# Optimization experiments

Measured on AMD Instinct MI355X. Metric: run time of the kernel, lower is better.

## Reference

```python
import jax, jax.numpy as jnp
import numpy as np

FACTOR = 3   # ProbAttention factor hardcoded in Informer.__init__
N_HEADS = 8


def _ln(x, g, b, eps=1e-5):
    m = x.mean(-1, keepdims=True)
    v = ((x - m) ** 2).mean(-1, keepdims=True)
    return (x - m) / jnp.sqrt(v + eps) * g + b


def _pos_emb(L, d_model):
    # standard fixed sinusoidal positional embedding (Informer PositionalEmbedding)
    pos = np.arange(L, dtype=np.float32)[:, None]
    div = np.exp(np.arange(0, d_model, 2, dtype=np.float32) * (-np.log(10000.0) / d_model))
    pe = np.zeros((L, d_model), np.float32)
    pe[:, 0::2] = np.sin(pos * div)
    pe[:, 1::2] = np.cos(pos * div)
    return jnp.asarray(pe)


def _prob_attention(q, k, v, rng_key):
    # q,k,v: [B, L, H, D]; mask_flag=False, scale=None -> 1/sqrt(D)
    B, L, H, D = q.shape
    Q = q.transpose(0, 2, 1, 3)
    K = k.transpose(0, 2, 1, 3)
    V = v.transpose(0, 2, 1, 3)
    L_Q = L_K = L
    U_part = min(FACTOR * int(np.ceil(np.log(L_K))), L_K)   # sampled keys per query
    u = min(FACTOR * int(np.ceil(np.log(L_Q))), L_Q)        # top queries kept
    # sample keys (shared across batch/heads, as in torch.randint(L_K,(L_Q,sample_k)))
    idx_sample = jax.random.randint(rng_key, (L_Q, U_part), 0, L_K)
    K_sample = K[:, :, idx_sample, :]                        # [B,H,L_Q,U_part,D]
    QK_sample = jnp.einsum('bhld,bhlsd->bhls', Q, K_sample)  # [B,H,L_Q,U_part]
    M = QK_sample.max(-1) - QK_sample.sum(-1) / L_K          # sparsity measure [B,H,L_Q]
    _, idx_top = jax.lax.top_k(M, u)                         # [B,H,u]
    Q_reduce = jnp.take_along_axis(Q, idx_top[..., None], axis=2)          # [B,H,u,D]
    scores = jnp.einsum('bhud,bhkd->bhuk', Q_reduce, K) / jnp.sqrt(jnp.float32(D))
    attn = jax.nn.softmax(scores, axis=-1)
    upd = jnp.einsum('bhuk,bhkd->bhud', attn, V)             # [B,H,u,D]
    # initial context = mean over values (mask_flag=False), overwrite at top queries
    ctx = jnp.broadcast_to(V.mean(axis=2, keepdims=True), (B, H, L_Q, D))
    bI = jnp.arange(B)[:, None, None]
    hI = jnp.arange(H)[None, :, None]
    ctx = ctx.at[bI, hI, idx_top].set(upd)
    return ctx.transpose(0, 2, 1, 3).reshape(B, L, H * D)


def _forward(x, time_features, g_in, b_in, W_tok, W_time, b_time,
             Wq, bq, Wk, bk, Wv, bv, Wo, bo, W1, b1, W2, b2,
             g1, be1, g2, be2, g_enc, b_enc, W_pre, b_pre, W_fc, b_fc):
    B, L, _ = x.shape
    d_model = W_tok.shape[-1]
    H = N_HEADS
    D = d_model // H
    x = _ln(x, g_in, b_in)                                   # input_norm over enc_in
    # DataEmbedding: circular Conv1d(k=3) token emb + positional + timeF linear
    xp = jnp.pad(x, ((0, 0), (1, 1), (0, 0)), mode='wrap')
    tok = jax.lax.conv_general_dilated(xp, W_tok, (1,), 'VALID',
                                       dimension_numbers=('NWC', 'WIO', 'NWC'))
    h = tok + _pos_emb(L, d_model)[None] + time_features @ W_time.T + b_time
    key = jax.random.key(42)
    for i in range(Wq.shape[0]):                              # e_layers (small, fixed)
        q = (h @ Wq[i].T + bq[i]).reshape(B, L, H, D)
        k = (h @ Wk[i].T + bk[i]).reshape(B, L, H, D)
        v = (h @ Wv[i].T + bv[i]).reshape(B, L, H, D)
        attn_out = _prob_attention(q, k, v, jax.random.fold_in(key, i))
        h = h + attn_out @ Wo[i].T + bo[i]
        h = _ln(h, g1[i], be1[i])
        y = jax.nn.relu(h @ W1[i].T + b1[i]) @ W2[i].T + b2[i]  # 1x1 convs == linears
        h = _ln(h + y, g2[i], be2[i])
    h = _ln(h, g_enc, b_enc)
    last = h[:, -1, :]
    return jax.nn.relu(last @ W_pre.T + b_pre) @ W_fc.T + b_fc


def setup_inputs() -> dict:
    key = jax.random.key(0)
    B, L, C_IN, DM, DFF, E = 8, 2048, 32, 512, 2048, 2
    ks = iter(jax.random.split(key, 48))

    def p(shape, s=0.02):
        return jax.random.normal(next(ks), shape, jnp.float32) * s

    return {
        'x': jax.random.normal(next(ks), (B, L, C_IN), jnp.float32),
        'time_features': jax.random.uniform(next(ks), (B, L, 4), jnp.float32),
        'g_in': jnp.ones((C_IN,), jnp.float32), 'b_in': jnp.zeros((C_IN,), jnp.float32),
        'W_tok': p((3, C_IN, DM)),
        'W_time': p((DM, 4)), 'b_time': jnp.zeros((DM,), jnp.float32),
        'Wq': p((E, DM, DM)), 'bq': jnp.zeros((E, DM), jnp.float32),
        'Wk': p((E, DM, DM)), 'bk': jnp.zeros((E, DM), jnp.float32),
        'Wv': p((E, DM, DM)), 'bv': jnp.zeros((E, DM), jnp.float32),
        'Wo': p((E, DM, DM)), 'bo': jnp.zeros((E, DM), jnp.float32),
        'W1': p((E, DFF, DM)), 'b1': jnp.zeros((E, DFF), jnp.float32),
        'W2': p((E, DM, DFF)), 'b2': jnp.zeros((E, DM), jnp.float32),
        'g1': jnp.ones((E, DM), jnp.float32), 'be1': jnp.zeros((E, DM), jnp.float32),
        'g2': jnp.ones((E, DM), jnp.float32), 'be2': jnp.zeros((E, DM), jnp.float32),
        'g_enc': jnp.ones((DM,), jnp.float32), 'b_enc': jnp.zeros((DM,), jnp.float32),
        'W_pre': p((DM // 2, DM)), 'b_pre': jnp.zeros((DM // 2,), jnp.float32),
        'W_fc': p((1, DM // 2)), 'b_fc': jnp.zeros((1,), jnp.float32),
    }


def reference(x, time_features, g_in, b_in, W_tok, W_time, b_time,
              Wq, bq, Wk, bk, Wv, bv, Wo, bo, W1, b1, W2, b2,
              g1, be1, g2, be2, g_enc, b_enc, W_pre, b_pre, W_fc, b_fc):
    return _forward(x, time_features, g_in, b_in, W_tok, W_time, b_time,
                    Wq, bq, Wk, bk, Wv, bv, Wo, bo, W1, b1, W2, b2,
                    g1, be1, g2, be2, g_enc, b_enc, W_pre, b_pre, W_fc, b_fc)
```

## Files before the change

### kernel.cpp

```cpp
#include <hip/hip_runtime.h>
#include <math.h>

#define BATCH 8
#define SEQ   2048
#define TOK   (BATCH*SEQ)
#define CIN   32
#define DM    512
#define DFF   2048
#define NH    8
#define HD    64
#define NSAMP 24
#define NTOP  24
#define NSLAB 8
#define EPS   1e-5f
#define QKVLD 1536

typedef unsigned int u32;
typedef unsigned short u16;
typedef unsigned long long u64;
typedef __attribute__((ext_vector_type(8))) short short8;
typedef __attribute__((ext_vector_type(4))) short short4v;
typedef __attribute__((ext_vector_type(4))) float floatx4;

__device__ __forceinline__ void async16(const void* g, void* l) {
    __builtin_amdgcn_global_load_lds((const __attribute__((address_space(1))) u32*)g,
                                     (__attribute__((address_space(3))) u32*)l, 16, 0, 0);
}
__device__ __forceinline__ u16 bf16rn(float f) {
    u32 u = __float_as_uint(f);
    return (u16)((u + 0x7fffu + ((u >> 16) & 1u)) >> 16);
}
__device__ __forceinline__ void sep_store(u16* base, size_t row, int ld2, int j, float v) {
    u16 hb = bf16rn(v);
    float r = v - __uint_as_float((u32)hb << 16);
    size_t o = row * (size_t)ld2 + (size_t)((j >> 3) << 4) + (j & 7);
    base[o] = hb;
    base[o + 8] = bf16rn(r);
}
__device__ __forceinline__ float sep_load(const u16* base, size_t row, int ld2, int j) {
    size_t o = row * (size_t)ld2 + (size_t)((j >> 3) << 4) + (j & 7);
    return __uint_as_float((u32)base[o] << 16) + __uint_as_float((u32)base[o + 8] << 16);
}
__device__ __forceinline__ float hl2f(u16 h, u16 l) {
    return __uint_as_float((u32)h << 16) + __uint_as_float((u32)l << 16);
}

__device__ __forceinline__ void tf_round(unsigned &x0, unsigned &x1, int r) {
    x0 += x1;
    x1 = (x1 << r) | (x1 >> (32 - r));
    x1 ^= x0;
}
__device__ __forceinline__ void threefry(unsigned k0, unsigned k1,
                                         unsigned c0, unsigned c1,
                                         unsigned &o0, unsigned &o1) {
    unsigned ks0 = k0, ks1 = k1, ks2 = k0 ^ k1 ^ 0x1BD11BDAu;
    unsigned x0 = c0 + ks0, x1 = c1 + ks1;
    tf_round(x0,x1,13); tf_round(x0,x1,15); tf_round(x0,x1,26); tf_round(x0,x1,6);
    x0 += ks1; x1 += ks2 + 1u;
    tf_round(x0,x1,17); tf_round(x0,x1,29); tf_round(x0,x1,16); tf_round(x0,x1,24);
    x0 += ks2; x1 += ks0 + 2u;
    tf_round(x0,x1,13); tf_round(x0,x1,15); tf_round(x0,x1,26); tf_round(x0,x1,6);
    x0 += ks0; x1 += ks1 + 3u;
    tf_round(x0,x1,17); tf_round(x0,x1,29); tf_round(x0,x1,16); tf_round(x0,x1,24);
    x0 += ks1; x1 += ks2 + 4u;
    tf_round(x0,x1,13); tf_round(x0,x1,15); tf_round(x0,x1,26); tf_round(x0,x1,6);
    x0 += ks2; x1 += ks0 + 5u;
    o0 = x0; o1 = x1;
}

__global__ void sample_kernel(int* __restrict__ idx_sample) {
    const int HALF = (SEQ * NSAMP) / 2;
    int p = blockIdx.x * blockDim.x + threadIdx.x;
    int li = blockIdx.y;
    if (p >= HALF) return;
    unsigned f0, f1;
    threefry(0u, 42u, 0u, (unsigned)li, f0, f1);
    unsigned a0, a1, b0, b1;
    threefry(f0, f1, 0u, 2u, a0, a1);
    threefry(f0, f1, 1u, 3u, b0, b1);
    unsigned o0, o1;
    threefry(a1, b1, (unsigned)p, (unsigned)(p + HALF), o0, o1);
    idx_sample[li * SEQ * NSAMP + p]        = (int)(o0 & (SEQ - 1));
    idx_sample[li * SEQ * NSAMP + p + HALF] = (int)(o1 & (SEQ - 1));
}

__global__ __launch_bounds__(256) void ln_in_kernel(const float* __restrict__ x,
        const float* __restrict__ g, const float* __restrict__ b,
        float* __restrict__ out) {
    int t = blockIdx.x * blockDim.x + threadIdx.x;
    if (t >= TOK) return;
    const float* xr = x + (size_t)t * CIN;
    float vals[CIN];
    float s = 0.f;
#pragma unroll
    for (int c = 0; c < CIN; c++) { vals[c] = xr[c]; s += vals[c]; }
    float m = s * (1.f / CIN);
    float v = 0.f;
#pragma unroll
    for (int c = 0; c < CIN; c++) { float d = vals[c] - m; v += d * d; }
    v *= (1.f / CIN);
    float inv = rsqrtf(v + EPS);
    float* orow = out + (size_t)t * CIN;
#pragma unroll
    for (int c = 0; c < CIN; c++) orow[c] = (vals[c] - m) * inv * g[c] + b[c];
}

__global__ __launch_bounds__(128) void im2col_kernel(const float* __restrict__ xln,
        u16* __restrict__ a) {
    int t = blockIdx.x;
    int j = threadIdx.x;
    if (j >= 96) return;
    int b = t >> 11, l = t & 2047;
    int w = j >> 5, c = j & 31;
    int lw = (l - 1 + w + SEQ) & 2047;
    sep_store(a, (size_t)t, 192, j, xln[(((size_t)b << 11) | lw) * CIN + c]);
}

__global__ __launch_bounds__(256) void wtok_split(const float* __restrict__ Wtok,
        u16* __restrict__ wt) {
    int e = blockIdx.x * 256 + threadIdx.x;
    int o = e / 96, j = e % 96;
    sep_store(wt, (size_t)o, 192, j, Wtok[(size_t)j * DM + o]);
}

__global__ __launch_bounds__(256) void pe_kernel(float* __restrict__ pe) {
    int e = blockIdx.x * 256 + threadIdx.x;
    int l = e >> 9, o = e & 511;
    const float c1 = -0.017988946039016f;
    int i2 = o & ~1;
    float div = expf((float)i2 * c1);
    float arg = (float)l * div;
    pe[e] = (o & 1) ? cosf(arg) : sinf(arg);
}

__global__ __launch_bounds__(256) void rsd_kernel(const float* __restrict__ pe,
        const float* __restrict__ tfeat, const float* __restrict__ Wtime,
        u16* __restrict__ rsd) {
    int t = blockIdx.x, tid = threadIdx.x;
    int l = t & 2047;
    float t0 = tfeat[(size_t)t * 4], t1 = tfeat[(size_t)t * 4 + 1];
    float t2 = tfeat[(size_t)t * 4 + 2], t3 = tfeat[(size_t)t * 4 + 3];
    for (int o = tid; o < DM; o += 256) {
        float v = pe[l * DM + o]
            + t0 * Wtime[o * 4] + t1 * Wtime[o * 4 + 1]
            + t2 * Wtime[o * 4 + 2] + t3 * Wtime[o * 4 + 3];
        sep_store(rsd, (size_t)t, 1024, o, v);
    }
}

__global__ __launch_bounds__(256) void split_weights(const float* __restrict__ Wq,
        const float* __restrict__ Wk, const float* __restrict__ Wv,
        const float* __restrict__ Wo, const float* __restrict__ W1,
        const float* __restrict__ W2, u16* __restrict__ out,
        const float* __restrict__ bq, const float* __restrict__ bk,
        const float* __restrict__ bv, float* __restrict__ bqkv) {
    int i = blockIdx.x * 256 + threadIdx.x;
    if (i < 1536)
        bqkv[i] = (i < 512) ? bq[i] : (i < 1024) ? bk[i - 512] : bv[i - 1024];
    if (i < 1048576) {
        const float* src = (i < 262144) ? Wq : (i < 524288) ? Wk : (i < 786432) ? Wv : Wo;
        int off = i & 262143;
        size_t base = (size_t)(i >> 18) * 524288;
        sep_store(out + base, (size_t)(off >> 9), 1024, off & 511, src[off]);
    } else if (i < 2097152) {
        int off = i - 1048576;
        sep_store(out + 2097152, (size_t)(off >> 9), 1024, off & 511, W1[off]);
    } else {
        int off = i - 2097152;
        sep_store(out + 4194304, (size_t)(off >> 11), 4096, off & 2047, W2[off]);
    }
}

template<bool RELU, bool RESP, bool OUTP, bool OUTB>
__global__ __launch_bounds__(256, 2) void gemm_pp(const u16* __restrict__ Ap,
        const u16* __restrict__ Wp, const float* __restrict__ bias,
        const u16* __restrict__ RsdS, float* __restrict__ Cf, u16* __restrict__ Cp,
        int ldc, int K, int lda) {
    __shared__ alignas(16) u16 At[2][8192];
    __shared__ alignas(16) u16 Wt[2][8192];
    const int tid = threadIdx.x;
    int linear = blockIdx.y * gridDim.x + blockIdx.x;
    int xcd = linear & 7, sseq = linear >> 3;
    int mper = gridDim.y >> 3;
    int mt = xcd * mper + (sseq % mper);
    int nt = sseq / mper;
    const int m0 = mt * 128, n0 = nt * 128;
    const int lane = tid & 63, wv = tid >> 6;
    const int wm = wv >> 1, wn = wv & 1;
    const int fr = lane & 15, q = lane >> 4;

    floatx4 acc[4][4] = {};

    const int r0 = tid >> 3;
    const int gc = (tid & 7) ^ (r0 & 7);
    const u16* abase = Ap + (size_t)(m0 + r0) * (2 * lda) + gc * 8;
    const u16* wbase = Wp + (size_t)(n0 + r0) * (2 * K) + gc * 8;
    const size_t astep = (size_t)32 * 2 * lda;
    const size_t wstep = (size_t)32 * 2 * K;
    const int doff = tid * 16;
    const int nk = K >> 5;

    const int cph = ((q << 1) ^ (fr & 7)) << 3;
    const int cpl = ((q << 1) ^ (fr & 7) ^ 1) << 3;

#pragma unroll
    for (int i = 0; i < 4; i++) {
        async16(abase + i * astep, (char*)At[0] + doff + i * 4096);
        async16(wbase + i * wstep, (char*)Wt[0] + doff + i * 4096);
    }

    for (int k = 0; k < nk; k++) {
        const int b = k & 1;
        __syncthreads();
        if (k + 1 < nk) {
            int k2 = (k + 1) << 6;
#pragma unroll
            for (int i = 0; i < 4; i++) {
                async16(abase + k2 + i * astep, (char*)At[b ^ 1] + doff + i * 4096);
                async16(wbase + k2 + i * wstep, (char*)Wt[b ^ 1] + doff + i * 4096);
            }
        }
        short8 ah[4], al[4];
#pragma unroll
        for (int mi = 0; mi < 4; mi++) {
            int r = wm * 64 + mi * 16 + fr;
            ah[mi] = *(const short8*)&At[b][r * 64 + cph];
            al[mi] = *(const short8*)&At[b][r * 64 + cpl];
        }
#pragma unroll
        for (int ni = 0; ni < 4; ni++) {
            int r = wn * 64 + ni * 16 + fr;
            short8 wh8 = *(const short8*)&Wt[b][r * 64 + cph];
            short8 wl8 = *(const short8*)&Wt[b][r * 64 + cpl];
#pragma unroll
            for (int mi = 0; mi < 4; mi++) {
                acc[mi][ni] = __builtin_amdgcn_mfma_f32_16x16x32_bf16(ah[mi], wh8, acc[mi][ni], 0, 0, 0);
                acc[mi][ni] = __builtin_amdgcn_mfma_f32_16x16x32_bf16(ah[mi], wl8, acc[mi][ni], 0, 0, 0);
                acc[mi][ni] = __builtin_amdgcn_mfma_f32_16x16x32_bf16(al[mi], wh8, acc[mi][ni], 0, 0, 0);
            }
        }
    }
#pragma unroll
    for (int ni = 0; ni < 4; ni++) {
        int col = n0 + wn * 64 + ni * 16 + fr;
        float bv = bias[col];
#pragma unroll
        for (int mi = 0; mi < 4; mi++) {
            int row = m0 + wm * 64 + mi * 16 + q * 4;
#pragma unroll
            for (int r = 0; r < 4; r++) {
                float v = acc[mi][ni][r] + bv;
                if (RESP) v += sep_load(RsdS, (size_t)(row + r), 2 * ldc, col);
                if (RELU) v = fmaxf(v, 0.f);
                if (OUTP)      sep_store(Cp, (size_t)(row + r), 2 * ldc, col, v);
                else if (OUTB) Cp[(size_t)(row + r) * ldc + col] = bf16rn(v);
                else           Cf[(size_t)(row + r) * ldc + col] = v;
            }
        }
    }
}

template<bool RELU, bool RESP>
__global__ __launch_bounds__(256, 2) void gemm_sb(const u16* __restrict__ Ab,
        const u16* __restrict__ Wp, const float* __restrict__ bias,
        const u16* __restrict__ RsdS, float* __restrict__ Cf,
        int ldc, int K, int lda) {
    __shared__ alignas(16) u16 At[2][4096];
    __shared__ alignas(16) u16 Wt[2][8192];
    const int tid = threadIdx.x;
    int linear = blockIdx.y * gridDim.x + blockIdx.x;
    int xcd = linear & 7, sseq = linear >> 3;
    int mper = gridDim.y >> 3;
    int mt = xcd * mper + (sseq % mper);
    int nt = sseq / mper;
    const int m0 = mt * 128, n0 = nt * 128;
    const int lane = tid & 63, wv = tid >> 6;
    const int wm = wv >> 1, wn = wv & 1;
    const int fr = lane & 15, q = lane >> 4;

    floatx4 acc[4][4] = {};

    const int ar = tid & 127;
    const u16* abase = Ab + (size_t)(m0 + ar) * lda + (tid >> 7) * 8;
    const int adoff = tid * 16;
    const int r0 = tid >> 3;
    const int gc = (tid & 7) ^ (r0 & 7);
    const u16* wbase = Wp + (size_t)(n0 + r0) * (2 * K) + gc * 8;
    const size_t wstep = (size_t)32 * 2 * K;
    const int wdoff = tid * 16;
    const int nk = K >> 5;

    const int cph = ((q << 1) ^ (fr & 7)) << 3;
    const int cpl = ((q << 1) ^ (fr & 7) ^ 1) << 3;

#pragma unroll
    for (int i = 0; i < 2; i++)
        async16(abase + i * 16, (char*)At[0] + adoff + i * 4096);
#pragma unroll
    for (int i = 0; i < 4; i++)
        async16(wbase + i * wstep, (char*)Wt[0] + wdoff + i * 4096);

    for (int k = 0; k < nk; k++) {
        const int b = k & 1;
        __syncthreads();
        if (k + 1 < nk) {
            int ka = (k + 1) << 5;
            int kw = (k + 1) << 6;
#pragma unroll
            for (int i = 0; i < 2; i++)
                async16(abase + ka + i * 16, (char*)At[b ^ 1] + adoff + i * 4096);
#pragma unroll
            for (int i = 0; i < 4; i++)
                async16(wbase + kw + i * wstep, (char*)Wt[b ^ 1] + wdoff + i * 4096);
        }
        short8 af[4];
#pragma unroll
        for (int mi = 0; mi < 4; mi++) {
            int r = wm * 64 + mi * 16 + fr;
            af[mi] = *(const short8*)&At[b][q * 1024 + r * 8];
        }
#pragma unroll
        for (int ni = 0; ni < 4; ni++) {
            int r = wn * 64 + ni * 16 + fr;
            short8 wh8 = *(const short8*)&Wt[b][r * 64 + cph];
            short8 wl8 = *(const short8*)&Wt[b][r * 64 + cpl];
#pragma unroll
            for (int mi = 0; mi < 4; mi++) {
                acc[mi][ni] = __builtin_amdgcn_mfma_f32_16x16x32_bf16(af[mi], wh8, acc[mi][ni], 0, 0, 0);
                acc[mi][ni] = __builtin_amdgcn_mfma_f32_16x16x32_bf16(af[mi], wl8, acc[mi][ni], 0, 0, 0);
            }
        }
    }
#pragma unroll
    for (int ni = 0; ni < 4; ni++) {
        int col = n0 + wn * 64 + ni * 16 + fr;
        float bv = bias[col];
#pragma unroll
        for (int mi = 0; mi < 4; mi++) {
            int row = m0 + wm * 64 + mi * 16 + q * 4;
#pragma unroll
            for (int r = 0; r < 4; r++) {
                float v = acc[mi][ni][r] + bv;
                if (RESP) v += sep_load(RsdS, (size_t)(row + r), 2 * ldc, col);
                if (RELU) v = fmaxf(v, 0.f);
                Cf[(size_t)(row + r) * ldc + col] = v;
            }
        }
    }
}

__global__ __launch_bounds__(256) void qk_sample_kernel(const float* __restrict__ qkv,
        const int* __restrict__ idx_sample, float* __restrict__ Mout) {
    int r = (blockIdx.x * 256 + threadIdx.x) >> 6;
    int lane = threadIdx.x & 63;
    if (r >= BATCH * NH * SEQ) return;
    int b = r / (NH * SEQ);
    int head = (r / SEQ) % NH;
    int l = r % SEQ;
    int sidx = lane >> 4, dc = lane & 15;
    const float* qrow = qkv + ((size_t)(b * SEQ + l)) * QKVLD + head * HD + dc * 4;
    float4 qf = *(const float4*)qrow;
    int myidx = (lane < NSAMP) ? idx_sample[l * NSAMP + lane] : 0;
    const float* kbase = qkv + (size_t)b * SEQ * QKVLD + 512 + head * HD + dc * 4;
    int kidx[6];
#pragma unroll
    for (int p = 0; p < 6; p++) kidx[p] = __shfl(myidx, p * 4 + sidx);
    float4 kf[6];
#pragma unroll
    for (int p = 0; p < 6; p++) kf[p] = *(const float4*)(kbase + (size_t)kidx[p] * QKVLD);
    float mx = -INFINITY, sm = 0.f;
#pragma unroll
    for (int p = 0; p < 6; p++) {
        float part = qf.x * kf[p].x + qf.y * kf[p].y + qf.z * kf[p].z + qf.w * kf[p].w;
        part += __shfl_xor(part, 1);
        part += __shfl_xor(part, 2);
        part += __shfl_xor(part, 4);
        part += __shfl_xor(part, 8);
        mx = fmaxf(mx, part);
        sm += part;
    }
    mx = fmaxf(mx, __shfl_xor(mx, 16));
    mx = fmaxf(mx, __shfl_xor(mx, 32));
    sm += __shfl_xor(sm, 16);
    sm += __shfl_xor(sm, 32);
    if (lane == 0) Mout[r] = mx - sm * (1.f / SEQ);
}

__device__ __forceinline__ u64 pack_key(float v, int idx) {
    u32 u = __float_as_uint(v);
    u32 m = (u & 0x80000000u) ? ~u : (u | 0x80000000u);
    return ((u64)m << 32) | (u32)(~(u32)idx);
}

__global__ __launch_bounds__(256) void topk_part(const float* __restrict__ Mbuf,
        u64* __restrict__ cand) {
    __shared__ u64 wred[4];
    int bh = blockIdx.x, chunk = blockIdx.y;
    int tid = threadIdx.x, wv = tid >> 6, lane = tid & 63;
    int l = chunk * 256 + tid;
    u64 val = pack_key(Mbuf[(size_t)bh * SEQ + l], l);
    for (int it = 0; it < NTOP; it++) {
        u64 w = val;
#pragma unroll
        for (int off = 32; off > 0; off >>= 1) {
            u64 o = __shfl_xor(w, off);
            if (o > w) w = o;
        }
        if (lane == 0) wred[wv] = w;
        __syncthreads();
        u64 win = wred[0];
        if (wred[1] > win) win = wred[1];
        if (wred[2] > win) win = wred[2];
        if (wred[3] > win) win = wred[3];
        if (val == win) val = 0;
        if (tid == 0) cand[((size_t)bh * 8 + chunk) * NTOP + it] = win;
        __syncthreads();
    }
}

__global__ __launch_bounds__(256) void topk_merge(const u64* __restrict__ cand,
        int* __restrict__ idx_top) {
    __shared__ u64 wred[4];
    int bh = blockIdx.x;
    int tid = threadIdx.x, wv = tid >> 6, lane = tid & 63;
    u64 val = (tid < 8 * NTOP) ? cand[(size_t)bh * 8 * NTOP + tid] : 0;
    for (int it = 0; it < NTOP; it++) {
        u64 w = val;
#pragma unroll
        for (int off = 32; off > 0; off >>= 1) {
            u64 o = __shfl_xor(w, off);
            if (o > w) w = o;
        }
        if (lane == 0) wred[wv] = w;
        __syncthreads();
        u64 win = wred[0];
        if (wred[1] > win) win = wred[1];
        if (wred[2] > win) win = wred[2];
        if (wred[3] > win) win = wred[3];
        if (val == win) val = 0;
        if (tid == 0) idx_top[bh * NTOP + it] = (int)(~(u32)(win & 0xffffffffull) & (SEQ - 1));
        __syncthreads();
    }
}

__global__ __launch_bounds__(256) void vmean_kernel(const float* __restrict__ qkv,
        float* __restrict__ vmean) {
    __shared__ float red[256];
    int bh = blockIdx.x, slab = blockIdx.y;
    int b = bh >> 3, head = bh & 7;
    int seg = threadIdx.x >> 6, d = threadIdx.x & 63;
    int base_row = slab * 256 + seg * 64;
    float s = 0.f;
    for (int r = 0; r < 64; r++)
        s += qkv[((size_t)(b * SEQ + base_row + r)) * QKVLD + 1024 + head * HD + d];
    red[threadIdx.x] = s;
    __syncthreads();
    if (threadIdx.x < 128) red[threadIdx.x] += red[threadIdx.x + 128];
    __syncthreads();
    if (threadIdx.x < 64) {
        float t = red[threadIdx.x] + red[threadIdx.x + 64];
        atomicAdd(&vmean[bh * HD + d], t * (1.f / SEQ));
    }
}

__global__ __launch_bounds__(512) void ydef_kernel(const float* __restrict__ Wo,
        const float* __restrict__ bo, const float* __restrict__ vmean,
        float* __restrict__ ydef) {
    __shared__ float vm[DM];
    int b = blockIdx.x, o = threadIdx.x;
    vm[o] = vmean[b * DM + o];
    __syncthreads();
    const float* wr = Wo + (size_t)o * DM;
    float acc = bo[o];
    for (int j = 0; j < DM; j += 4) {
        float4 w4 = *(const float4*)&wr[j];
        acc += w4.x * vm[j] + w4.y * vm[j + 1] + w4.z * vm[j + 2] + w4.w * vm[j + 3];
    }
    ydef[b * DM + o] = acc;
}

__global__ __launch_bounds__(256) void resid_kernel(const u16* __restrict__ hp,
        const float* __restrict__ ydef, float* __restrict__ hf) {
    int wv = threadIdx.x >> 6, lane = threadIdx.x & 63;
    int t = blockIdx.x * 4 + wv;
    int b = t >> 11;
    const u16* sp = hp + (size_t)t * 1024 + (lane >> 1) * 16 + (lane & 1) * 4;
    short4v h0 = *(const short4v*)sp;
    short4v l0 = *(const short4v*)(sp + 8);
    short4v h1 = *(const short4v*)(sp + 512);
    short4v l1 = *(const short4v*)(sp + 520);
    int j0 = (lane >> 1) * 8 + (lane & 1) * 4;
    const float* yd = ydef + b * DM;
    float4 y0 = *(const float4*)&yd[j0];
    float4 y1 = *(const float4*)&yd[j0 + 256];
    float4 o0, o1;
    o0.x = hl2f((u16)h0[0], (u16)l0[0]) + y0.x;
    o0.y = hl2f((u16)h0[1], (u16)l0[1]) + y0.y;
    o0.z = hl2f((u16)h0[2], (u16)l0[2]) + y0.z;
    o0.w = hl2f((u16)h0[3], (u16)l0[3]) + y0.w;
    o1.x = hl2f((u16)h1[0], (u16)l1[0]) + y1.x;
    o1.y = hl2f((u16)h1[1], (u16)l1[1]) + y1.y;
    o1.z = hl2f((u16)h1[2], (u16)l1[2]) + y1.z;
    o1.w = hl2f((u16)h1[3], (u16)l1[3]) + y1.w;
    *(float4*)&hf[(size_t)t * DM + j0] = o0;
    *(float4*)&hf[(size_t)t * DM + j0 + 256] = o1;
}

__global__ __launch_bounds__(512) void corr_kernel(const float* __restrict__ Wo,
        const float* __restrict__ updC, const float* __restrict__ vmean,
        const int* __restrict__ idx_top, float* __restrict__ hf) {
    __shared__ float delta[NTOP][HD];
    __shared__ int rows[NTOP];
    int bh = blockIdx.x, b = bh >> 3, h = bh & 7;
    int tid = threadIdx.x;
    for (int i = tid; i < NTOP * HD; i += 512) {
        int u = i >> 6, d = i & 63;
        delta[u][d] = updC[((size_t)bh * NTOP + u) * HD + d] - vmean[bh * HD + d];
    }
    if (tid < NTOP) rows[tid] = idx_top[bh * NTOP + tid];
    __syncthreads();
    float w[HD];
    const float* wr = Wo + (size_t)tid * DM + h * HD;
#pragma unroll
    for (int d = 0; d < HD; d += 4) {
        float4 f = *(const float4*)&wr[d];
        w[d] = f.x; w[d + 1] = f.y; w[d + 2] = f.z; w[d + 3] = f.w;
    }
    for (int u = 0; u < NTOP; u++) {
        float acc = 0.f;
#pragma unroll
        for (int d = 0; d < HD; d++) acc += w[d] * delta[u][d];
        atomicAdd(&hf[(size_t)(b * SEQ + rows[u]) * DM + tid], acc);
    }
}

__global__ __launch_bounds__(256) void spattn_flash(const float* __restrict__ qkv,
        const int* __restrict__ idx_top, float* __restrict__ opart,
        float* __restrict__ mspart) {
    __shared__ float KtT[64][65];
    __shared__ float Vt[64][65];
    __shared__ float Qs[24][64];
    __shared__ float Ps[24][66];
    int bh = blockIdx.x, slab = blockIdx.y;
    int b = bh >> 3, h = bh & 7;
    int tid = threadIdx.x;
    int wv = tid >> 6, lane = tid & 63;
    for (int i = tid; i < NTOP * 64; i += 256) {
        int u = i >> 6, d = i & 63;
        int qi = idx_top[bh * NTOP + u];
        Qs[u][d] = qkv[((size_t)(b * SEQ + qi)) * QKVLD + h * HD + d];
    }
    float m[6], s[6], o[6], alpha[6];
#pragma unroll
    for (int j = 0; j < 6; j++) { m[j] = -INFINITY; s[j] = 0.f; o[j] = 0.f; }
    int key0 = slab * (SEQ / NSLAB);
    int sr = tid >> 2, sc0 = (tid & 3) * 16;
    for (int t = 0; t < (SEQ / NSLAB) / 64; t++) {
        int kbase = key0 + t * 64;
        __syncthreads();
        const float* kr = qkv + ((size_t)(b * SEQ + kbase + sr)) * QKVLD + 512 + h * HD + sc0;
        const float* vr = qkv + ((size_t)(b * SEQ + kbase + sr)) * QKVLD + 1024 + h * HD + sc0;
        float kf[16], vf[16];
        *(float4*)&kf[0]  = *(const float4*)(kr);
        *(float4*)&kf[4]  = *(const float4*)(kr + 4);
        *(float4*)&kf[8]  = *(const float4*)(kr + 8);
        *(float4*)&kf[12] = *(const float4*)(kr + 12);
        *(float4*)&vf[0]  = *(const float4*)(vr);
        *(float4*)&vf[4]  = *(const float4*)(vr + 4);
        *(float4*)&vf[8]  = *(const float4*)(vr + 8);
        *(float4*)&vf[12] = *(const float4*)(vr + 12);
#pragma unroll
        for (int i = 0; i < 16; i++) {
            KtT[sc0 + i][sr] = kf[i];
            Vt[sr][sc0 + i] = vf[i];
        }
        __syncthreads();
        float dot[6] = {};
#pragma unroll
        for (int d = 0; d < 64; d++) {
            float kv = KtT[d][lane];
#pragma unroll
            for (int j = 0; j < 6; j++) dot[j] += Qs[wv * 6 + j][d] * kv;
        }
#pragma unroll
        for (int j = 0; j < 6; j++) {
            float sc = dot[j] * 0.125f;
            float tmax = sc;
            for (int off = 32; off > 0; off >>= 1) tmax = fmaxf(tmax, __shfl_xor(tmax, off));
            float mn = fmaxf(m[j], tmax);
            float p = __expf(sc - mn);
            float psum = p;
            for (int off = 32; off > 0; off >>= 1) psum += __shfl_xor(psum, off);
            alpha[j] = __expf(m[j] - mn);
            s[j] = s[j] * alpha[j] + psum;
            m[j] = mn;
            Ps[wv * 6 + j][lane] = p;
        }
        float pv[6] = {};
#pragma unroll
        for (int key = 0; key < 64; key++) {
            float vvv = Vt[key][lane];
#pragma unroll
            for (int j = 0; j < 6; j++) pv[j] += Ps[wv * 6 + j][key] * vvv;
        }
#pragma unroll
        for (int j = 0; j < 6; j++) o[j] = o[j] * alpha[j] + pv[j];
    }
    float* ob = opart + ((size_t)(bh * NSLAB + slab)) * NTOP * 64;
#pragma unroll
    for (int j = 0; j < 6; j++) ob[(wv * 6 + j) * 64 + lane] = o[j];
    if (lane == 0) {
        float* ms = mspart + ((size_t)(bh * NSLAB + slab)) * NTOP * 2;
#pragma unroll
        for (int j = 0; j < 6; j++) {
            ms[(wv * 6 + j) * 2]     = m[j];
            ms[(wv * 6 + j) * 2 + 1] = s[j];
        }
    }
}

__global__ __launch_bounds__(256) void spattn_combine(const float* __restrict__ opart,
        const float* __restrict__ mspart, float* __restrict__ updC) {
    __shared__ float wgt[NSLAB][NTOP];
    int bh = blockIdx.x;
    int tid = threadIdx.x;
    if (tid < NTOP) {
        float mv[NSLAB], sv[NSLAB];
        float M = -INFINITY;
#pragma unroll
        for (int sl = 0; sl < NSLAB; sl++) {
            mv[sl] = mspart[((size_t)(bh * NSLAB + sl)) * NTOP * 2 + tid * 2];
            sv[sl] = mspart[((size_t)(bh * NSLAB + sl)) * NTOP * 2 + tid * 2 + 1];
            M = fmaxf(M, mv[sl]);
        }
        float S = 0.f;
#pragma unroll
        for (int sl = 0; sl < NSLAB; sl++) S += sv[sl] * __expf(mv[sl] - M);
        float invS = 1.f / S;
#pragma unroll
        for (int sl = 0; sl < NSLAB; sl++) wgt[sl][tid] = __expf(mv[sl] - M) * invS;
    }
    __syncthreads();
    for (int i = tid; i < NTOP * 64; i += 256) {
        int u = i >> 6, d = i & 63;
        float val = 0.f;
#pragma unroll
        for (int sl = 0; sl < NSLAB; sl++)
            val += wgt[sl][u] * opart[(((size_t)(bh * NSLAB + sl)) * NTOP + u) * 64 + d];
        updC[((size_t)bh * NTOP + u) * 64 + d] = val;
    }
}

template<bool INP, bool OUTSEP>
__global__ __launch_bounds__(256) void ln_kernel(const float* __restrict__ srcF,
        const u16* __restrict__ srcS, const float* __restrict__ g,
        const float* __restrict__ b, float* __restrict__ dstF, u16* __restrict__ dstS) {
    int wv = threadIdx.x >> 6, lane = threadIdx.x & 63;
    int t = blockIdx.x * 4 + wv;
    float xv[8];
    if (INP) {
        const u16* sp = srcS + (size_t)t * 1024 + (lane >> 1) * 16 + (lane & 1) * 4;
        short4v h0 = *(const short4v*)sp;
        short4v l0 = *(const short4v*)(sp + 8);
        short4v h1 = *(const short4v*)(sp + 512);
        short4v l1 = *(const short4v*)(sp + 520);
#pragma unroll
        for (int i = 0; i < 4; i++) {
            xv[i]     = hl2f((u16)h0[i], (u16)l0[i]);
            xv[i + 4] = hl2f((u16)h1[i], (u16)l1[i]);
        }
    } else {
        float4 x0 = *(const float4*)&srcF[(size_t)t * DM + lane * 4];
        float4 x1 = *(const float4*)&srcF[(size_t)t * DM + lane * 4 + 256];
        xv[0] = x0.x; xv[1] = x0.y; xv[2] = x0.z; xv[3] = x0.w;
        xv[4] = x1.x; xv[5] = x1.y; xv[6] = x1.z; xv[7] = x1.w;
    }
    float s = 0.f, s2 = 0.f;
#pragma unroll
    for (int i = 0; i < 8; i++) { s += xv[i]; s2 += xv[i] * xv[i]; }
#pragma unroll
    for (int off = 32; off > 0; off >>= 1) {
        s  += __shfl_xor(s, off);
        s2 += __shfl_xor(s2, off);
    }
    float m = s * (1.f / DM);
    float var = s2 * (1.f / DM) - m * m;
    float inv = rsqrtf(var + EPS);
    float4 g0 = *(const float4*)&g[lane * 4];
    float4 g1 = *(const float4*)&g[lane * 4 + 256];
    float4 b0 = *(const float4*)&b[lane * 4];
    float4 b1 = *(const float4*)&b[lane * 4 + 256];
    float y[8];
    y[0] = (xv[0] - m) * inv * g0.x + b0.x;  y[1] = (xv[1] - m) * inv * g0.y + b0.y;
    y[2] = (xv[2] - m) * inv * g0.z + b0.z;  y[3] = (xv[3] - m) * inv * g0.w + b0.w;
    y[4] = (xv[4] - m) * inv * g1.x + b1.x;  y[5] = (xv[5] - m) * inv * g1.y + b1.y;
    y[6] = (xv[6] - m) * inv * g1.z + b1.z;  y[7] = (xv[7] - m) * inv * g1.w + b1.w;
    if (OUTSEP) {
        u16* dp = dstS + (size_t)t * 1024 + (lane >> 1) * 16 + (lane & 1) * 4;
        short4v hh0, ll0, hh1, ll1;
#pragma unroll
        for (int i = 0; i < 4; i++) {
            u16 hb = bf16rn(y[i]);
            hh0[i] = (short)hb;
            ll0[i] = (short)bf16rn(y[i] - __uint_as_float((u32)hb << 16));
            u16 hb2 = bf16rn(y[i + 4]);
            hh1[i] = (short)hb2;
            ll1[i] = (short)bf16rn(y[i + 4] - __uint_as_float((u32)hb2 << 16));
        }
        *(short4v*)dp = hh0;
        *(short4v*)(dp + 8) = ll0;
        *(short4v*)(dp + 512) = hh1;
        *(short4v*)(dp + 520) = ll1;
    } else {
        float4 o0 = { y[0], y[1], y[2], y[3] };
        float4 o1 = { y[4], y[5], y[6], y[7] };
        *(float4*)&dstF[(size_t)t * DM + lane * 4] = o0;
        *(float4*)&dstF[(size_t)t * DM + lane * 4 + 256] = o1;
    }
}

__global__ __launch_bounds__(256) void head_kernel(const float* __restrict__ hfin,
        const float* __restrict__ Wpre, const float* __restrict__ bpre,
        const float* __restrict__ Wfc, const float* __restrict__ bfc,
        float* __restrict__ out) {
    __shared__ float last[DM];
    __shared__ float red[256];
    int b = blockIdx.x, tid = threadIdx.x;
    const float* hr = hfin + ((size_t)(b * SEQ + SEQ - 1)) * DM;
    last[tid] = hr[tid];
    last[tid + 256] = hr[tid + 256];
    __syncthreads();
    float acc = bpre[tid];
    for (int c = 0; c < DM; c++) acc += last[c] * Wpre[tid * DM + c];
    acc = fmaxf(acc, 0.f);
    red[tid] = acc * Wfc[tid];
    __syncthreads();
    for (int s = 128; s > 0; s >>= 1) { if (tid < s) red[tid] += red[tid + s]; __syncthreads(); }
    if (tid == 0) out[b] = red[0] + bfc[0];
}

extern "C" void kernel_launch(void* const* d_in, const int* in_sizes, int n_in,
                              void* d_out, int out_size, void* d_ws, size_t ws_size,
                              hipStream_t stream) {
    (void)in_sizes; (void)n_in; (void)out_size; (void)ws_size;
    const float* x      = (const float*)d_in[0];
    const float* tfeat  = (const float*)d_in[1];
    const float* g_in   = (const float*)d_in[2];
    const float* b_in   = (const float*)d_in[3];
    const float* W_tok  = (const float*)d_in[4];
    const float* W_time = (const float*)d_in[5];
    const float* b_time = (const float*)d_in[6];
    const float* Wq     = (const float*)d_in[7];
    const float* bq     = (const float*)d_in[8];
    const float* Wk     = (const float*)d_in[9];
    const float* bk     = (const float*)d_in[10];
    const float* Wv     = (const float*)d_in[11];
    const float* bv     = (const float*)d_in[12];
    const float* Wo     = (const float*)d_in[13];
    const float* bo     = (const float*)d_in[14];
    const float* W1     = (const float*)d_in[15];
    const float* b1     = (const float*)d_in[16];
    const float* W2     = (const float*)d_in[17];
    const float* b2     = (const float*)d_in[18];
    const float* g1     = (const float*)d_in[19];
    const float* be1    = (const float*)d_in[20];
    const float* g2     = (const float*)d_in[21];
    const float* be2    = (const float*)d_in[22];
    const float* g_enc  = (const float*)d_in[23];
    const float* b_enc  = (const float*)d_in[24];
    const float* W_pre  = (const float*)d_in[25];
    const float* b_pre  = (const float*)d_in[26];
    const float* W_fc   = (const float*)d_in[27];
    const float* b_fc   = (const float*)d_in[28];
    float* out = (float*)d_out;

    char* ws = (char*)d_ws;
    u16*   hp   = (u16*)(ws);
    float* hf   = (float*)(ws + 33554432);
    char*  bigc = ws + 67108864;
    float* qkv  = (float*)bigc;
    u16*   midP = (u16*)bigc;
    u16*   midB = (u16*)bigc;
    float* updC   = (float*)(bigc + 100663296);
    float* ydefb  = (float*)(bigc + 101056512);
    float* opart  = (float*)(bigc + 101072896);
    float* mspart = (float*)(bigc + 104218624);
    float* xln  = (float*)(bigc);
    u16*   acvP = (u16*)(bigc + 2097152);
    float* pe   = (float*)(bigc + 8388608);
    u16*   rsdS = (u16*)(bigc + 12582912);
    u16*   wtok = (u16*)(bigc + 46137344);
    u16*   wsep       = (u16*)(ws + 201326592);
    float* Mbuf       = (float*)(ws + 213909504);
    float* vmean      = (float*)(ws + 214433792);
    int*   idx_sample = (int*)(ws + 214450176);
    int*   idx_top    = (int*)(ws + 214843392);
    float* biasqkv    = (float*)(ws + 214849536);
    u64*   cand       = (u64*)(ws + 214855680);

    ln_in_kernel<<<TOK / 256, 256, 0, stream>>>(x, g_in, b_in, xln);
    im2col_kernel<<<TOK, 128, 0, stream>>>(xln, acvP);
    wtok_split<<<192, 256, 0, stream>>>(W_tok, wtok);
    pe_kernel<<<4096, 256, 0, stream>>>(pe);
    rsd_kernel<<<TOK, 256, 0, stream>>>(pe, tfeat, W_time, rsdS);
    sample_kernel<<<dim3(96, 2), 256, 0, stream>>>(idx_sample);

    gemm_pp<false, true, true, false><<<dim3(4, 128), 256, 0, stream>>>(
        acvP, wtok, b_time, rsdS, nullptr, hp, DM, 96, 96);

    const u16* wqkv_p = wsep;
    const u16* w1_p = wsep + 2097152;
    const u16* w2_p = wsep + 4194304;

    for (int li = 0; li < 2; li++) {
        split_weights<<<12288, 256, 0, stream>>>(
            Wq + (size_t)li * DM * DM, Wk + (size_t)li * DM * DM,
            Wv + (size_t)li * DM * DM, Wo + (size_t)li * DM * DM,
            W1 + (size_t)li * DFF * DM, W2 + (size_t)li * DM * DFF, wsep,
            bq + (size_t)li * DM, bk + (size_t)li * DM, bv + (size_t)li * DM, biasqkv);

        const float* Wo_i = Wo + (size_t)li * DM * DM;
        const float* bo_i = bo + (size_t)li * DM;
        const float* b1_i = b1 + (size_t)li * DFF;
        const float* b2_i = b2 + (size_t)li * DM;
        const float* g1_i = g1 + (size_t)li * DM;
        const float* be1_i = be1 + (size_t)li * DM;
        const float* g2_i = g2 + (size_t)li * DM;
        const float* be2_i = be2 + (size_t)li * DM;

        gemm_pp<false, false, false, false><<<dim3(QKVLD / 128, TOK / 128), 256, 0, stream>>>(
            hp, wqkv_p, biasqkv, nullptr, qkv, nullptr, QKVLD, DM, DM);

        qk_sample_kernel<<<(BATCH * NH * SEQ) / 4, 256, 0, stream>>>(
            qkv, idx_sample + li * SEQ * NSAMP, Mbuf);
        topk_part<<<dim3(BATCH * NH, 8), 256, 0, stream>>>(Mbuf, cand);
        topk_merge<<<BATCH * NH, 256, 0, stream>>>(cand, idx_top);
        hipMemsetAsync(vmean, 0, BATCH * NH * HD * sizeof(float), stream);
        vmean_kernel<<<dim3(BATCH * NH, 8), 256, 0, stream>>>(qkv, vmean);
        ydef_kernel<<<BATCH, 512, 0, stream>>>(Wo_i, bo_i, vmean, ydefb);
        spattn_flash<<<dim3(BATCH * NH, NSLAB), 256, 0, stream>>>(qkv, idx_top, opart, mspart);
        spattn_combine<<<BATCH * NH, 256, 0, stream>>>(opart, mspart, updC);

        resid_kernel<<<TOK / 4, 256, 0, stream>>>(hp, ydefb, hf);
        corr_kernel<<<BATCH * NH, 512, 0, stream>>>(Wo_i, updC, vmean, idx_top, hf);
        ln_kernel<false, true><<<TOK / 4, 256, 0, stream>>>(hf, nullptr, g1_i, be1_i, nullptr, hp);

        if (li == 0) {
            gemm_pp<true, false, true, false><<<dim3(DFF / 128, TOK / 128), 256, 0, stream>>>(
                hp, w1_p, b1_i, nullptr, nullptr, midP, DFF, DM, DM);
            gemm_pp<false, true, false, false><<<dim3(DM / 128, TOK / 128), 256, 0, stream>>>(
                midP, w2_p, b2_i, hp, hf, nullptr, DM, DFF, DFF);
        } else {
            gemm_pp<true, false, false, true><<<dim3(DFF / 128, TOK / 128), 256, 0, stream>>>(
                hp, w1_p, b1_i, nullptr, nullptr, midB, DFF, DM, DM);
            gemm_sb<false, true><<<dim3(DM / 128, TOK / 128), 256, 0, stream>>>(
                midB, w2_p, b2_i, hp, hf, DM, DFF, DFF);
        }
        ln_kernel<false, true><<<TOK / 4, 256, 0, stream>>>(hf, nullptr, g2_i, be2_i, nullptr, hp);
    }

    ln_kernel<true, false><<<TOK / 4, 256, 0, stream>>>(nullptr, hp, g_enc, b_enc, hf, nullptr);
    head_kernel<<<BATCH, 256, 0, stream>>>(hf, W_pre, b_pre, W_fc, b_fc, out);
}
```

Measured before the change: 1.131 ms.

## Fuse residual, sparse-attention correction and LayerNorm; fold V-mean into attention kernel

Merges the input LayerNorm and im2col into one warp-shuffle kernel. Computes the V mean inside the sparse flash-attention kernel instead of a separate pass over V. Replaces the resid, atomic corr and LayerNorm kernels with one fused pass driven by a per-token head mask and top-query map, which avoids the hf round trip and the atomics. This adds bookkeeping buffers and a memset, and the fused LayerNorm uses the one-pass variance formula, which is less numerically robust.

```diff
diff --git a/kernel.cpp b/kernel.cpp
--- a/kernel.cpp
+++ b/kernel.cpp
@@ -84,36 +84,27 @@
     idx_sample[li * SEQ * NSAMP + p + HALF] = (int)(o1 & (SEQ - 1));
 }
 
-__global__ __launch_bounds__(256) void ln_in_kernel(const float* __restrict__ x,
-        const float* __restrict__ g, const float* __restrict__ b,
-        float* __restrict__ out) {
-    int t = blockIdx.x * blockDim.x + threadIdx.x;
-    if (t >= TOK) return;
-    const float* xr = x + (size_t)t * CIN;
-    float vals[CIN];
-    float s = 0.f;
-#pragma unroll
-    for (int c = 0; c < CIN; c++) { vals[c] = xr[c]; s += vals[c]; }
-    float m = s * (1.f / CIN);
-    float v = 0.f;
-#pragma unroll
-    for (int c = 0; c < CIN; c++) { float d = vals[c] - m; v += d * d; }
-    v *= (1.f / CIN);
-    float inv = rsqrtf(v + EPS);
-    float* orow = out + (size_t)t * CIN;
-#pragma unroll
-    for (int c = 0; c < CIN; c++) orow[c] = (vals[c] - m) * inv * g[c] + b[c];
-}
-
-__global__ __launch_bounds__(128) void im2col_kernel(const float* __restrict__ xln,
-        u16* __restrict__ a) {
-    int t = blockIdx.x;
-    int j = threadIdx.x;
-    if (j >= 96) return;
-    int b = t >> 11, l = t & 2047;
-    int w = j >> 5, c = j & 31;
-    int lw = (l - 1 + w + SEQ) & 2047;
-    sep_store(a, (size_t)t, 192, j, xln[(((size_t)b << 11) | lw) * CIN + c]);
+__global__ __launch_bounds__(256) void ln_im2col_kernel(const float* __restrict__ x,
+        const float* __restrict__ g, const float* __restrict__ b, u16* __restrict__ a) {
+    int sub = threadIdx.x >> 5;
+    int c   = threadIdx.x & 31;
+    int t = blockIdx.x * 8 + sub;
+    int bb = t >> 11, l = t & 2047;
+    float v = x[(size_t)t * CIN + c];
+    float s = v;
+#pragma unroll
+    for (int m = 1; m <= 16; m <<= 1) s += __shfl_xor(s, m);
+    float mean = s * (1.f / CIN);
+    float d = v - mean;
+    float vv = d * d;
+#pragma unroll
+    for (int m = 1; m <= 16; m <<= 1) vv += __shfl_xor(vv, m);
+    float inv = rsqrtf(vv * (1.f / CIN) + EPS);
+    float y = d * inv * g[c] + b[c];
+    size_t base = (size_t)(bb << 11);
+    sep_store(a, base + ((l + 1) & 2047), 192, c, y);
+    sep_store(a, base + l,                192, 32 + c, y);
+    sep_store(a, base + ((l - 1) & 2047), 192, 64 + c, y);
 }
 
 __global__ __launch_bounds__(256) void wtok_split(const float* __restrict__ Wtok,
@@ -419,7 +410,7 @@
 }
 
 __global__ __launch_bounds__(256) void topk_merge(const u64* __restrict__ cand,
-        int* __restrict__ idx_top) {
+        int* __restrict__ idx_top, u32* __restrict__ headmask, u16* __restrict__ umap) {
     __shared__ u64 wred[4];
     int bh = blockIdx.x;
     int tid = threadIdx.x, wv = tid >> 6, lane = tid & 63;
@@ -438,28 +429,13 @@
         if (wred[2] > win) win = wred[2];
         if (wred[3] > win) win = wred[3];
         if (val == win) val = 0;
-        if (tid == 0) idx_top[bh * NTOP + it] = (int)(~(u32)(win & 0xffffffffull) & (SEQ - 1));
+        if (tid == 0) {
+            int row = (int)(~(u32)(win & 0xffffffffull) & (SEQ - 1));
+            idx_top[bh * NTOP + it] = row;
+            umap[(size_t)bh * SEQ + row] = (u16)it;
+            atomicOr(&headmask[(((bh >> 3) << 11) | row)], 1u << (bh & 7));
+        }
         __syncthreads();
-    }
-}
-
-__global__ __launch_bounds__(256) void vmean_kernel(const float* __restrict__ qkv,
-        float* __restrict__ vmean) {
-    __shared__ float red[256];
-    int bh = blockIdx.x, slab = blockIdx.y;
-    int b = bh >> 3, head = bh & 7;
-    int seg = threadIdx.x >> 6, d = threadIdx.x & 63;
-    int base_row = slab * 256 + seg * 64;
-    float s = 0.f;
-    for (int r = 0; r < 64; r++)
-        s += qkv[((size_t)(b * SEQ + base_row + r)) * QKVLD + 1024 + head * HD + d];
-    red[threadIdx.x] = s;
-    __syncthreads();
-    if (threadIdx.x < 128) red[threadIdx.x] += red[threadIdx.x + 128];
-    __syncthreads();
-    if (threadIdx.x < 64) {
-        float t = red[threadIdx.x] + red[threadIdx.x + 64];
-        atomicAdd(&vmean[bh * HD + d], t * (1.f / SEQ));
     }
 }
 
@@ -479,68 +455,115 @@
     ydef[b * DM + o] = acc;
 }
 
-__global__ __launch_bounds__(256) void resid_kernel(const u16* __restrict__ hp,
-        const float* __restrict__ ydef, float* __restrict__ hf) {
+__global__ __launch_bounds__(512) void corrRow_kernel(const float* __restrict__ Wo,
+        const float* __restrict__ updC, const float* __restrict__ vmean,
+        float* __restrict__ corrRow) {
+    __shared__ float delta[NTOP][HD];
+    int bh = blockIdx.x, h = bh & 7;
+    int tid = threadIdx.x;
+    for (int i = tid; i < NTOP * HD; i += 512) {
+        int u = i >> 6, d = i & 63;
+        delta[u][d] = updC[((size_t)bh * NTOP + u) * HD + d] - vmean[bh * HD + d];
+    }
+    __syncthreads();
+    float w[HD];
+    const float* wr = Wo + (size_t)tid * DM + h * HD;
+#pragma unroll
+    for (int d = 0; d < HD; d += 4) {
+        float4 f = *(const float4*)&wr[d];
+        w[d] = f.x; w[d + 1] = f.y; w[d + 2] = f.z; w[d + 3] = f.w;
+    }
+    for (int u = 0; u < NTOP; u++) {
+        float acc = 0.f;
+#pragma unroll
+        for (int d = 0; d < HD; d++) acc += w[d] * delta[u][d];
+        corrRow[((size_t)bh * NTOP + u) * DM + tid] = acc;
+    }
+}
+
+__global__ __launch_bounds__(256) void resid_corr_ln(const u16* __restrict__ hp,
+        const float* __restrict__ ydef, const float* __restrict__ corrRow,
+        const u32* __restrict__ headmask, const u16* __restrict__ umap,
+        const float* __restrict__ g, const float* __restrict__ b,
+        u16* __restrict__ dstS) {
     int wv = threadIdx.x >> 6, lane = threadIdx.x & 63;
     int t = blockIdx.x * 4 + wv;
-    int b = t >> 11;
+    int bb = t >> 11, l = t & 2047;
     const u16* sp = hp + (size_t)t * 1024 + (lane >> 1) * 16 + (lane & 1) * 4;
     short4v h0 = *(const short4v*)sp;
     short4v l0 = *(const short4v*)(sp + 8);
     short4v h1 = *(const short4v*)(sp + 512);
     short4v l1 = *(const short4v*)(sp + 520);
     int j0 = (lane >> 1) * 8 + (lane & 1) * 4;
-    const float* yd = ydef + b * DM;
+    const float* yd = ydef + bb * DM;
     float4 y0 = *(const float4*)&yd[j0];
     float4 y1 = *(const float4*)&yd[j0 + 256];
-    float4 o0, o1;
-    o0.x = hl2f((u16)h0[0], (u16)l0[0]) + y0.x;
-    o0.y = hl2f((u16)h0[1], (u16)l0[1]) + y0.y;
-    o0.z = hl2f((u16)h0[2], (u16)l0[2]) + y0.z;
-    o0.w = hl2f((u16)h0[3], (u16)l0[3]) + y0.w;
-    o1.x = hl2f((u16)h1[0], (u16)l1[0]) + y1.x;
-    o1.y = hl2f((u16)h1[1], (u16)l1[1]) + y1.y;
-    o1.z = hl2f((u16)h1[2], (u16)l1[2]) + y1.z;
-    o1.w = hl2f((u16)h1[3], (u16)l1[3]) + y1.w;
-    *(float4*)&hf[(size_t)t * DM + j0] = o0;
-    *(float4*)&hf[(size_t)t * DM + j0 + 256] = o1;
-}
-
-__global__ __launch_bounds__(512) void corr_kernel(const float* __restrict__ Wo,
-        const float* __restrict__ updC, const float* __restrict__ vmean,
-        const int* __restrict__ idx_top, float* __restrict__ hf) {
-    __shared__ float delta[NTOP][HD];
-    __shared__ int rows[NTOP];
-    int bh = blockIdx.x, b = bh >> 3, h = bh & 7;
-    int tid = threadIdx.x;
-    for (int i = tid; i < NTOP * HD; i += 512) {
-        int u = i >> 6, d = i & 63;
-        delta[u][d] = updC[((size_t)bh * NTOP + u) * HD + d] - vmean[bh * HD + d];
-    }
-    if (tid < NTOP) rows[tid] = idx_top[bh * NTOP + tid];
-    __syncthreads();
-    float w[HD];
-    const float* wr = Wo + (size_t)tid * DM + h * HD;
-#pragma unroll
-    for (int d = 0; d < HD; d += 4) {
-        float4 f = *(const float4*)&wr[d];
-        w[d] = f.x; w[d + 1] = f.y; w[d + 2] = f.z; w[d + 3] = f.w;
-    }
-    for (int u = 0; u < NTOP; u++) {
-        float acc = 0.f;
-#pragma unroll
-        for (int d = 0; d < HD; d++) acc += w[d] * delta[u][d];
-        atomicAdd(&hf[(size_t)(b * SEQ + rows[u]) * DM + tid], acc);
-    }
+    float xv[8];
+    xv[0] = hl2f((u16)h0[0], (u16)l0[0]) + y0.x;
+    xv[1] = hl2f((u16)h0[1], (u16)l0[1]) + y0.y;
+    xv[2] = hl2f((u16)h0[2], (u16)l0[2]) + y0.z;
+    xv[3] = hl2f((u16)h0[3], (u16)l0[3]) + y0.w;
+    xv[4] = hl2f((u16)h1[0], (u16)l1[0]) + y1.x;
+    xv[5] = hl2f((u16)h1[1], (u16)l1[1]) + y1.y;
+    xv[6] = hl2f((u16)h1[2], (u16)l1[2]) + y1.z;
+    xv[7] = hl2f((u16)h1[3], (u16)l1[3]) + y1.w;
+    u32 mask = headmask[t];
+    while (mask) {
+        int h = __ffs(mask) - 1;
+        mask &= mask - 1;
+        int bh = bb * NH + h;
+        int u = umap[(size_t)bh * SEQ + l];
+        const float* cr = corrRow + ((size_t)bh * NTOP + u) * DM;
+        float4 c0 = *(const float4*)&cr[j0];
+        float4 c1 = *(const float4*)&cr[j0 + 256];
+        xv[0] += c0.x; xv[1] += c0.y; xv[2] += c0.z; xv[3] += c0.w;
+        xv[4] += c1.x; xv[5] += c1.y; xv[6] += c1.z; xv[7] += c1.w;
+    }
+    float s = 0.f, s2 = 0.f;
+#pragma unroll
+    for (int i = 0; i < 8; i++) { s += xv[i]; s2 += xv[i] * xv[i]; }
+#pragma unroll
+    for (int off = 32; off > 0; off >>= 1) {
+        s  += __shfl_xor(s, off);
+        s2 += __shfl_xor(s2, off);
+    }
+    float m = s * (1.f / DM);
+    float var = s2 * (1.f / DM) - m * m;
+    float inv = rsqrtf(var + EPS);
+    float4 g0 = *(const float4*)&g[lane * 4];
+    float4 g1 = *(const float4*)&g[lane * 4 + 256];
+    float4 b0 = *(const float4*)&b[lane * 4];
+    float4 b1 = *(const float4*)&b[lane * 4 + 256];
+    float y[8];
+    y[0] = (xv[0] - m) * inv * g0.x + b0.x;  y[1] = (xv[1] - m) * inv * g0.y + b0.y;
+    y[2] = (xv[2] - m) * inv * g0.z + b0.z;  y[3] = (xv[3] - m) * inv * g0.w + b0.w;
+    y[4] = (xv[4] - m) * inv * g1.x + b1.x;  y[5] = (xv[5] - m) * inv * g1.y + b1.y;
+    y[6] = (xv[6] - m) * inv * g1.z + b1.z;  y[7] = (xv[7] - m) * inv * g1.w + b1.w;
+    u16* dp = dstS + (size_t)t * 1024 + (lane >> 1) * 16 + (lane & 1) * 4;
+    short4v hh0, ll0, hh1, ll1;
+#pragma unroll
+    for (int i = 0; i < 4; i++) {
+        u16 hb = bf16rn(y[i]);
+        hh0[i] = (short)hb;
+        ll0[i] = (short)bf16rn(y[i] - __uint_as_float((u32)hb << 16));
+        u16 hb2 = bf16rn(y[i + 4]);
+        hh1[i] = (short)hb2;
+        ll1[i] = (short)bf16rn(y[i + 4] - __uint_as_float((u32)hb2 << 16));
+    }
+    *(short4v*)dp = hh0;
+    *(short4v*)(dp + 8) = ll0;
+    *(short4v*)(dp + 512) = hh1;
+    *(short4v*)(dp + 520) = ll1;
 }
 
 __global__ __launch_bounds__(256) void spattn_flash(const float* __restrict__ qkv,
         const int* __restrict__ idx_top, float* __restrict__ opart,
-        float* __restrict__ mspart) {
+        float* __restrict__ mspart, float* __restrict__ vmean) {
     __shared__ float KtT[64][65];
     __shared__ float Vt[64][65];
     __shared__ float Qs[24][64];
     __shared__ float Ps[24][66];
+    __shared__ float vred[4][4][16];
     int bh = blockIdx.x, slab = blockIdx.y;
     int b = bh >> 3, h = bh & 7;
     int tid = threadIdx.x;
@@ -553,6 +576,9 @@
     float m[6], s[6], o[6], alpha[6];
 #pragma unroll
     for (int j = 0; j < 6; j++) { m[j] = -INFINITY; s[j] = 0.f; o[j] = 0.f; }
+    float vacc[16];
+#pragma unroll
+    for (int i = 0; i < 16; i++) vacc[i] = 0.f;
     int key0 = slab * (SEQ / NSLAB);
     int sr = tid >> 2, sc0 = (tid & 3) * 16;
     for (int t = 0; t < (SEQ / NSLAB) / 64; t++) {
@@ -573,6 +599,7 @@
         for (int i = 0; i < 16; i++) {
             KtT[sc0 + i][sr] = kf[i];
             Vt[sr][sc0 + i] = vf[i];
+            vacc[i] += vf[i];
         }
         __syncthreads();
         float dot[6] = {};
@@ -616,6 +643,20 @@
             ms[(wv * 6 + j) * 2]     = m[j];
             ms[(wv * 6 + j) * 2 + 1] = s[j];
         }
+    }
+#pragma unroll
+    for (int mm = 4; mm <= 32; mm <<= 1)
+#pragma unroll
+        for (int i = 0; i < 16; i++) vacc[i] += __shfl_xor(vacc[i], mm);
+    if ((lane >> 2) == 0) {
+#pragma unroll
+        for (int i = 0; i < 16; i++) vred[wv][lane & 3][i] = vacc[i];
+    }
+    __syncthreads();
+    if (tid < 64) {
+        int g4 = tid >> 4, i = tid & 15;
+        float s4 = vred[0][g4][i] + vred[1][g4][i] + vred[2][g4][i] + vred[3][g4][i];
+        atomicAdd(&vmean[bh * HD + tid], s4 * (1.f / SEQ));
     }
 }
 
@@ -781,25 +822,26 @@
     float* qkv  = (float*)bigc;
     u16*   midP = (u16*)bigc;
     u16*   midB = (u16*)bigc;
-    float* updC   = (float*)(bigc + 100663296);
-    float* ydefb  = (float*)(bigc + 101056512);
-    float* opart  = (float*)(bigc + 101072896);
-    float* mspart = (float*)(bigc + 104218624);
-    float* xln  = (float*)(bigc);
+    float* updC    = (float*)(bigc + 100663296);
+    float* ydefb   = (float*)(bigc + 101056512);
+    float* opart   = (float*)(bigc + 101072896);
+    float* mspart  = (float*)(bigc + 104218624);
+    float* corrRow = (float*)(bigc + 104316928);
+    float* vmeanN  = (float*)(bigc + 107462656);
+    u32*   headmask= (u32*)(bigc + 107479040);
+    u16*   umap    = (u16*)(bigc + 107544576);
     u16*   acvP = (u16*)(bigc + 2097152);
     float* pe   = (float*)(bigc + 8388608);
     u16*   rsdS = (u16*)(bigc + 12582912);
     u16*   wtok = (u16*)(bigc + 46137344);
     u16*   wsep       = (u16*)(ws + 201326592);
     float* Mbuf       = (float*)(ws + 213909504);
-    float* vmean      = (float*)(ws + 214433792);
     int*   idx_sample = (int*)(ws + 214450176);
     int*   idx_top    = (int*)(ws + 214843392);
     float* biasqkv    = (float*)(ws + 214849536);
     u64*   cand       = (u64*)(ws + 214855680);
 
-    ln_in_kernel<<<TOK / 256, 256, 0, stream>>>(x, g_in, b_in, xln);
-    im2col_kernel<<<TOK, 128, 0, stream>>>(xln, acvP);
+    ln_im2col_kernel<<<TOK / 8, 256, 0, stream>>>(x, g_in, b_in, acvP);
     wtok_split<<<192, 256, 0, stream>>>(W_tok, wtok);
     pe_kernel<<<4096, 256, 0, stream>>>(pe);
     rsd_kernel<<<TOK, 256, 0, stream>>>(pe, tfeat, W_time, rsdS);
@@ -834,16 +876,16 @@
         qk_sample_kernel<<<(BATCH * NH * SEQ) / 4, 256, 0, stream>>>(
             qkv, idx_sample + li * SEQ * NSAMP, Mbuf);
         topk_part<<<dim3(BATCH * NH, 8), 256, 0, stream>>>(Mbuf, cand);
-        topk_merge<<<BATCH * NH, 256, 0, stream>>>(cand, idx_top);
-        hipMemsetAsync(vmean, 0, BATCH * NH * HD * sizeof(float), stream);
-        vmean_kernel<<<dim3(BATCH * NH, 8), 256, 0, stream>>>(qkv, vmean);
-        ydef_kernel<<<BATCH, 512, 0, stream>>>(Wo_i, bo_i, vmean, ydefb);
-        spattn_flash<<<dim3(BATCH * NH, NSLAB), 256, 0, stream>>>(qkv, idx_top, opart, mspart);
+        hipMemsetAsync(vmeanN, 0, 16384 + 65536, stream);
+        topk_merge<<<BATCH * NH, 256, 0, stream>>>(cand, idx_top, headmask, umap);
+        spattn_flash<<<dim3(BATCH * NH, NSLAB), 256, 0, stream>>>(
+            qkv, idx_top, opart, mspart, vmeanN);
         spattn_combine<<<BATCH * NH, 256, 0, stream>>>(opart, mspart, updC);
-
-        resid_kernel<<<TOK / 4, 256, 0, stream>>>(hp, ydefb, hf);
-        corr_kernel<<<BATCH * NH, 512, 0, stream>>>(Wo_i, updC, vmean, idx_top, hf);
-        ln_kernel<false, true><<<TOK / 4, 256, 0, stream>>>(hf, nullptr, g1_i, be1_i, nullptr, hp);
+        ydef_kernel<<<BATCH, 512, 0, stream>>>(Wo_i, bo_i, vmeanN, ydefb);
+        corrRow_kernel<<<BATCH * NH, 512, 0, stream>>>(Wo_i, updC, vmeanN, corrRow);
+
+        resid_corr_ln<<<TOK / 4, 256, 0, stream>>>(
+            hp, ydefb, corrRow, headmask, umap, g1_i, be1_i, hp);
 
         if (li == 0) {
             gemm_pp<true, false, true, false><<<dim3(DFF / 128, TOK / 128), 256, 0, stream>>>(
```

After: 1.139 ms. Within noise of the previous version (+0.7%).
